# Optimization experiments

Hardware: AMD Instinct MI355X
Metric: run time of the kernel (lower is better)

The kernel has to match this reference:

```python
import jax, jax.numpy as jnp
import numpy as np

ETYPES = [0, 2, 1]          # indexes into doubled RotatE0 r_vec (2*R rows)
OUT_DIM = 64
NUM_HEADS = 8
ALPHA = 0.01                # LeakyReLU slope
R = 2                       # raw relation count (r_vec rows before doubling)
N = 100000                  # num nodes
E = 250000                  # num edges (metapath instances)
L = len(ETYPES) + 1         # metapath length


def setup_inputs() -> dict:
    key = jax.random.key(0)
    k = jax.random.split(key, 6)
    features = jax.random.normal(k[0], (N, OUT_DIM), jnp.float32)
    r_vec = jax.random.normal(k[1], (R, OUT_DIM // 2, 2), jnp.float32)
    attn1_w = jax.random.normal(k[2], (NUM_HEADS, OUT_DIM), jnp.float32) * 0.1
    attn2 = jax.random.normal(k[3], (1, NUM_HEADS, OUT_DIM), jnp.float32) * 0.1
    edge_metapath_indices = jax.random.randint(k[4], (E, L), 0, N)
    edge_dst = jax.random.randint(k[5], (E,), 0, N)
    return {"features": features, "r_vec": r_vec, "attn1_w": attn1_w,
            "attn2": attn2, "edge_metapath_indices": edge_metapath_indices,
            "edge_dst": edge_dst}


def _forward(features, r_vec, attn1_w, attn2, edge_metapath_indices, edge_dst):
    D2 = OUT_DIM // 2
    # --- RotatE0 relation vectors: normalize each complex pair to unit length ---
    rv = r_vec / jnp.linalg.norm(r_vec, axis=2, keepdims=True)      # [R, D2, 2]
    rv_conj = rv * jnp.array([1.0, -1.0], rv.dtype)                 # conjugate
    rv2 = jnp.stack((rv, rv_conj), axis=1).reshape(2 * R, D2, 2)    # [2R, D2, 2]
    # --- cumulative rotation per metapath position (reverse product) ---
    fr = [None] * L
    fr[L - 1] = jnp.stack([jnp.ones(D2, rv.dtype), jnp.zeros(D2, rv.dtype)], -1)
    for i in range(L - 2, -1, -1):
        if ETYPES[i] is not None:
            r = rv2[ETYPES[i]]                                       # [D2, 2]
            re = fr[i + 1][:, 0] * r[:, 0] - fr[i + 1][:, 1] * r[:, 1]
            im = fr[i + 1][:, 0] * r[:, 1] + fr[i + 1][:, 1] * r[:, 0]
            fr[i] = jnp.stack([re, im], axis=-1)
        else:
            fr[i] = fr[i + 1]
    frv = jnp.stack(fr, axis=0)                                      # [L, D2, 2]
    # --- gather node features along each metapath instance ---
    edata = features[edge_metapath_indices]                          # [E, L, D]
    ed = edata.reshape(edata.shape[0], L, D2, 2)
    # position L-1 has identity rotation (1,0), so rotate all positions at once
    re = ed[..., 0] * frv[None, :, :, 0] - ed[..., 1] * frv[None, :, :, 1]
    im = ed[..., 0] * frv[None, :, :, 1] + ed[..., 1] * frv[None, :, :, 0]
    ed = jnp.stack([re, im], axis=-1).reshape(edata.shape[0], L, OUT_DIM)
    hidden = ed.mean(axis=1)                                         # [E, D]
    eft = jnp.tile(hidden, (1, NUM_HEADS)).reshape(-1, NUM_HEADS, OUT_DIM)
    # --- attention scores (attn_switch=True) ---
    center = features[edge_metapath_indices[:, -1]]                  # [E, D]
    a1 = center @ attn1_w.T                                          # [E, H]
    a2 = (eft * attn2).sum(axis=-1)                                  # [E, H]
    a = a1 + a2
    a = jnp.where(a > 0, a, ALPHA * a)[:, :, None]                   # leaky relu, [E,H,1]
    # --- edge softmax over destination-node segments ---
    amax = jax.lax.stop_gradient(jax.ops.segment_max(a, edge_dst, num_segments=N))
    aexp = jnp.exp(a - amax[edge_dst])
    asum = jax.ops.segment_sum(aexp, edge_dst, num_segments=N)
    attn = aexp / asum[edge_dst]                                     # [E, H, 1]
    # --- message passing: weighted scatter-sum to destination nodes ---
    h = jax.ops.segment_sum(eft * attn, edge_dst, num_segments=N)    # [N, H, D]
    return h


def reference(features, r_vec, attn1_w, attn2, edge_metapath_indices, edge_dst):
    return _forward(features, r_vec, attn1_w, attn2, edge_metapath_indices, edge_dst)
```

## Files before the change

kernel.cpp:

```cpp
#include <hip/hip_runtime.h>

#define NUM_HEADS 8

__device__ __forceinline__ float2 cmul(float2 a, float2 b) {
    return make_float2(a.x*b.x - a.y*b.y, a.x*b.y + a.y*b.x);
}

__global__ __launch_bounds__(256) void k_edge(
    const float2* __restrict__ feat,
    const float2* __restrict__ rvec,
    const float2* __restrict__ w1_g,
    const float2* __restrict__ w2_g,
    const int4*   __restrict__ emi,
    const int*    __restrict__ edge_dst,
    float2*       __restrict__ hidden,
    float*        __restrict__ a_buf,
    int*          __restrict__ counts,
    int E)
{
    __shared__ float2 s_frv[96];
    __shared__ float2 s_w1[256];
    __shared__ float2 s_w2[256];
    int tid = threadIdx.x;
    if (tid < 32) {
        float2 a = rvec[tid];
        float2 b = rvec[32 + tid];
        float na = rsqrtf(a.x*a.x + a.y*a.y); a.x *= na; a.y *= na;
        float nb = rsqrtf(b.x*b.x + b.y*b.y); b.x *= nb; b.y *= nb;
        float2 fr2 = make_float2(a.x, -a.y);
        float2 fr1 = cmul(fr2, b);
        float2 fr0 = cmul(fr1, a);
        s_frv[tid] = fr0; s_frv[32+tid] = fr1; s_frv[64+tid] = fr2;
    }
    s_w1[tid] = w1_g[tid];
    s_w2[tid] = w2_g[tid];
    __syncthreads();

    int e = blockIdx.x * 8 + (tid >> 5);
    if (e >= E) return;
    int lane = tid & 31;

    int4 idx = emi[e];
    float2 f0 = feat[(size_t)idx.x * 32 + lane];
    float2 f1 = feat[(size_t)idx.y * 32 + lane];
    float2 f2 = feat[(size_t)idx.z * 32 + lane];
    float2 c3 = feat[(size_t)idx.w * 32 + lane];

    float2 acc = c3;
    float2 q;
    q = s_frv[lane];      acc.x += f0.x*q.x - f0.y*q.y; acc.y += f0.x*q.y + f0.y*q.x;
    q = s_frv[32+lane];   acc.x += f1.x*q.x - f1.y*q.y; acc.y += f1.x*q.y + f1.y*q.x;
    q = s_frv[64+lane];   acc.x += f2.x*q.x - f2.y*q.y; acc.y += f2.x*q.y + f2.y*q.x;
    float2 h = make_float2(acc.x * 0.25f, acc.y * 0.25f);
    hidden[(size_t)e * 32 + lane] = h;

    float p[NUM_HEADS];
    #pragma unroll
    for (int hh = 0; hh < NUM_HEADS; ++hh) {
        float2 w1 = s_w1[hh*32 + lane], w2 = s_w2[hh*32 + lane];
        p[hh] = c3.x*w1.x + c3.y*w1.y + h.x*w2.x + h.y*w2.y;
    }
    float myv = 0.f;
    #pragma unroll
    for (int hh = 0; hh < NUM_HEADS; ++hh) {
        #pragma unroll
        for (int off = 16; off > 0; off >>= 1)
            p[hh] += __shfl_xor(p[hh], off, 32);
        if (lane == hh) myv = p[hh];
    }
    if (lane < NUM_HEADS) {
        float a = myv > 0.f ? myv : 0.01f * myv;
        a_buf[(size_t)e * 8 + lane] = a;
    }
    if (lane == 0) atomicAdd(&counts[edge_dst[e]], 1);
}

__global__ __launch_bounds__(256) void k_scan_a(
    const int* __restrict__ counts, int* __restrict__ offsets,
    int* __restrict__ blocksums, int N)
{
    __shared__ int s[256];
    int t = threadIdx.x;
    int base = blockIdx.x * 1024 + t * 4;
    int v0 = (base     < N) ? counts[base]     : 0;
    int v1 = (base + 1 < N) ? counts[base + 1] : 0;
    int v2 = (base + 2 < N) ? counts[base + 2] : 0;
    int v3 = (base + 3 < N) ? counts[base + 3] : 0;
    s[t] = v0 + v1 + v2 + v3;
    __syncthreads();
    #pragma unroll
    for (int off = 1; off < 256; off <<= 1) {
        int x = (t >= off) ? s[t - off] : 0;
        __syncthreads();
        s[t] += x;
        __syncthreads();
    }
    if (t == 255) blocksums[blockIdx.x] = s[255];
    int run = (t == 0) ? 0 : s[t - 1];
    if (base     < N) offsets[base]     = run; run += v0;
    if (base + 1 < N) offsets[base + 1] = run; run += v1;
    if (base + 2 < N) offsets[base + 2] = run; run += v2;
    if (base + 3 < N) offsets[base + 3] = run;
}

__global__ __launch_bounds__(1024) void k_scan_b(
    int* __restrict__ blocksums, int* __restrict__ total, int B)
{
    __shared__ int s[1024];
    int t = threadIdx.x;
    s[t] = (t < B) ? blocksums[t] : 0;
    __syncthreads();
    #pragma unroll
    for (int off = 1; off < 1024; off <<= 1) {
        int x = (t >= off) ? s[t - off] : 0;
        __syncthreads();
        s[t] += x;
        __syncthreads();
    }
    if (t < B) blocksums[t] = (t == 0) ? 0 : s[t - 1];
    if (t == 1023) *total = s[1023];
}

__global__ __launch_bounds__(256) void k_scan_c(
    int* __restrict__ offsets, int* __restrict__ cursor,
    const int* __restrict__ blocksums, const int* __restrict__ total, int N)
{
    int i = blockIdx.x * 256 + threadIdx.x;
    if (i < N) {
        int v = offsets[i] + blocksums[i >> 10];
        offsets[i] = v;
        cursor[i] = v;
    }
    if (i == 0) offsets[N] = *total;
}

__global__ void k_fill(const int* __restrict__ edge_dst, int* __restrict__ cursor,
                       int* __restrict__ edge_ids, int E) {
    int e = blockIdx.x * 256 + threadIdx.x;
    if (e >= E) return;
    int pos = atomicAdd(&cursor[edge_dst[e]], 1);
    edge_ids[pos] = e;
}

__global__ __launch_bounds__(256) void k_out(
    const float2* __restrict__ hidden,
    const float*  __restrict__ a_buf,
    const int*    __restrict__ offsets,
    const int*    __restrict__ edge_ids,
    float2*       __restrict__ out,
    int N)
{
    int tid = threadIdx.x;
    int n = blockIdx.x * 8 + (tid >> 5);
    if (n >= N) return;
    int lane = tid & 31;
    int beg = offsets[n], end = offsets[n + 1];

    if (beg == end) {
        float2 z = make_float2(0.f, 0.f);
        #pragma unroll
        for (int hh = 0; hh < NUM_HEADS; ++hh)
            out[((size_t)n * 8 + hh) * 32 + lane] = z;
        return;
    }

    const float4* a4 = (const float4*)a_buf;
    float4 m0 = make_float4(-1e30f, -1e30f, -1e30f, -1e30f);
    float4 m1 = m0;
    for (int j = beg; j < end; ++j) {
        int e = edge_ids[j];
        float4 x0 = a4[(size_t)e * 2], x1 = a4[(size_t)e * 2 + 1];
        m0.x = fmaxf(m0.x, x0.x); m0.y = fmaxf(m0.y, x0.y);
        m0.z = fmaxf(m0.z, x0.z); m0.w = fmaxf(m0.w, x0.w);
        m1.x = fmaxf(m1.x, x1.x); m1.y = fmaxf(m1.y, x1.y);
        m1.z = fmaxf(m1.z, x1.z); m1.w = fmaxf(m1.w, x1.w);
    }
    float4 d0 = make_float4(0.f, 0.f, 0.f, 0.f), d1 = d0;
    float2 acc[NUM_HEADS];
    #pragma unroll
    for (int hh = 0; hh < NUM_HEADS; ++hh) acc[hh] = make_float2(0.f, 0.f);
    for (int j = beg; j < end; ++j) {
        int e = edge_ids[j];
        float4 x0 = a4[(size_t)e * 2], x1 = a4[(size_t)e * 2 + 1];
        float w0x = __expf(x0.x - m0.x), w0y = __expf(x0.y - m0.y);
        float w0z = __expf(x0.z - m0.z), w0w = __expf(x0.w - m0.w);
        float w1x = __expf(x1.x - m1.x), w1y = __expf(x1.y - m1.y);
        float w1z = __expf(x1.z - m1.z), w1w = __expf(x1.w - m1.w);
        d0.x += w0x; d0.y += w0y; d0.z += w0z; d0.w += w0w;
        d1.x += w1x; d1.y += w1y; d1.z += w1z; d1.w += w1w;
        float2 hv = hidden[(size_t)e * 32 + lane];
        acc[0].x += hv.x * w0x; acc[0].y += hv.y * w0x;
        acc[1].x += hv.x * w0y; acc[1].y += hv.y * w0y;
        acc[2].x += hv.x * w0z; acc[2].y += hv.y * w0z;
        acc[3].x += hv.x * w0w; acc[3].y += hv.y * w0w;
        acc[4].x += hv.x * w1x; acc[4].y += hv.y * w1x;
        acc[5].x += hv.x * w1y; acc[5].y += hv.y * w1y;
        acc[6].x += hv.x * w1z; acc[6].y += hv.y * w1z;
        acc[7].x += hv.x * w1w; acc[7].y += hv.y * w1w;
    }
    float r[NUM_HEADS] = {1.f/d0.x, 1.f/d0.y, 1.f/d0.z, 1.f/d0.w,
                          1.f/d1.x, 1.f/d1.y, 1.f/d1.z, 1.f/d1.w};
    #pragma unroll
    for (int hh = 0; hh < NUM_HEADS; ++hh) {
        float2 v = make_float2(acc[hh].x * r[hh], acc[hh].y * r[hh]);
        out[((size_t)n * 8 + hh) * 32 + lane] = v;
    }
}

extern "C" void kernel_launch(void* const* d_in, const int* in_sizes, int n_in,
                              void* d_out, int out_size, void* d_ws, size_t ws_size,
                              hipStream_t stream) {
    const float2* feat = (const float2*)d_in[0];
    const float2* rvec = (const float2*)d_in[1];
    const float2* w1   = (const float2*)d_in[2];
    const float2* w2   = (const float2*)d_in[3];
    const int4*   emi  = (const int4*)d_in[4];
    const int* edge_dst = (const int*)d_in[5];

    int N = in_sizes[0] / 64;
    int E = in_sizes[4] / 4;
    int nTiles = (N + 1023) / 1024;

    char* w = (char*)d_ws;
    float*    hidden   = (float*)w;
    float*    a_buf    = hidden + (size_t)E * 64;
    int*      counts   = (int*)(a_buf + (size_t)E * 8);
    int*      offsets  = counts + N;
    int*      cursor   = offsets + N + 1;
    int*      edge_ids = cursor + N;
    int*      blocksums= edge_ids + E;
    int*      total    = blocksums + 1024;

    hipMemsetAsync(counts, 0, (size_t)N * 4, stream);

    k_edge<<<(E + 7) / 8, 256, 0, stream>>>(feat, rvec, w1, w2, emi, edge_dst,
                                            (float2*)hidden, a_buf, counts, E);
    k_scan_a<<<nTiles, 256, 0, stream>>>(counts, offsets, blocksums, N);
    k_scan_b<<<1, 1024, 0, stream>>>(blocksums, total, nTiles);
    k_scan_c<<<(N + 255) / 256, 256, 0, stream>>>(offsets, cursor, blocksums, total, N);
    k_fill<<<(E + 255) / 256, 256, 0, stream>>>(edge_dst, cursor, edge_ids, E);
    k_out<<<(N + 7) / 8, 256, 0, stream>>>((const float2*)hidden, a_buf,
                                           offsets, edge_ids, (float2*)d_out, N);
}
```

Measured before the change: 376.4 us.

## Precompute per-node attention projections and fuse edge computation into the CSR gather kernel

```diff
diff --git a/kernel.cpp b/kernel.cpp
--- a/kernel.cpp
+++ b/kernel.cpp
@@ -6,73 +6,51 @@
     return make_float2(a.x*b.x - a.y*b.y, a.x*b.y + a.y*b.x);
 }
 
-__global__ __launch_bounds__(256) void k_edge(
+__global__ __launch_bounds__(256) void k_pre(
     const float2* __restrict__ feat,
     const float2* __restrict__ rvec,
     const float2* __restrict__ w1_g,
     const float2* __restrict__ w2_g,
-    const int4*   __restrict__ emi,
-    const int*    __restrict__ edge_dst,
-    float2*       __restrict__ hidden,
-    float*        __restrict__ a_buf,
-    int*          __restrict__ counts,
-    int E)
-{
-    __shared__ float2 s_frv[96];
-    __shared__ float2 s_w1[256];
-    __shared__ float2 s_w2[256];
+    float*        __restrict__ P, int N)
+{
     int tid = threadIdx.x;
-    if (tid < 32) {
-        float2 a = rvec[tid];
-        float2 b = rvec[32 + tid];
+    int lane = tid & 31;
+    int l = lane >> 3, h = lane & 7;
+
+    float2 Wr[32];
+    for (int d = 0; d < 32; ++d) {
+        float2 a = rvec[d], b = rvec[32 + d];
         float na = rsqrtf(a.x*a.x + a.y*a.y); a.x *= na; a.y *= na;
         float nb = rsqrtf(b.x*b.x + b.y*b.y); b.x *= nb; b.y *= nb;
         float2 fr2 = make_float2(a.x, -a.y);
         float2 fr1 = cmul(fr2, b);
         float2 fr0 = cmul(fr1, a);
-        s_frv[tid] = fr0; s_frv[32+tid] = fr1; s_frv[64+tid] = fr2;
-    }
-    s_w1[tid] = w1_g[tid];
-    s_w2[tid] = w2_g[tid];
-    __syncthreads();
-
-    int e = blockIdx.x * 8 + (tid >> 5);
-    if (e >= E) return;
-    int lane = tid & 31;
-
-    int4 idx = emi[e];
-    float2 f0 = feat[(size_t)idx.x * 32 + lane];
-    float2 f1 = feat[(size_t)idx.y * 32 + lane];
-    float2 f2 = feat[(size_t)idx.z * 32 + lane];
-    float2 c3 = feat[(size_t)idx.w * 32 + lane];
-
-    float2 acc = c3;
-    float2 q;
-    q = s_frv[lane];      acc.x += f0.x*q.x - f0.y*q.y; acc.y += f0.x*q.y + f0.y*q.x;
-    q = s_frv[32+lane];   acc.x += f1.x*q.x - f1.y*q.y; acc.y += f1.x*q.y + f1.y*q.x;
-    q = s_frv[64+lane];   acc.x += f2.x*q.x - f2.y*q.y; acc.y += f2.x*q.y + f2.y*q.x;
-    float2 h = make_float2(acc.x * 0.25f, acc.y * 0.25f);
-    hidden[(size_t)e * 32 + lane] = h;
-
-    float p[NUM_HEADS];
-    #pragma unroll
-    for (int hh = 0; hh < NUM_HEADS; ++hh) {
-        float2 w1 = s_w1[hh*32 + lane], w2 = s_w2[hh*32 + lane];
-        p[hh] = c3.x*w1.x + c3.y*w1.y + h.x*w2.x + h.y*w2.y;
-    }
-    float myv = 0.f;
-    #pragma unroll
-    for (int hh = 0; hh < NUM_HEADS; ++hh) {
+        float2 fr = (l == 0) ? fr0 : (l == 1) ? fr1 : (l == 2) ? fr2 : make_float2(1.f, 0.f);
+        float2 frc = make_float2(fr.x, -fr.y);
+        float2 w2 = w2_g[h*32 + d];
+        float2 wl = cmul(w2, frc);
+        wl.x *= 0.25f; wl.y *= 0.25f;
+        if (l == 3) { float2 w1 = w1_g[h*32 + d]; wl.x += w1.x; wl.y += w1.y; }
+        Wr[d] = wl;
+    }
+
+    int g = tid >> 5;
+    for (int n = blockIdx.x * 8 + g; n < N; n += gridDim.x * 8) {
+        const float4* f4 = (const float4*)(feat + (size_t)n * 32);
+        float acc = 0.f;
         #pragma unroll
-        for (int off = 16; off > 0; off >>= 1)
-            p[hh] += __shfl_xor(p[hh], off, 32);
-        if (lane == hh) myv = p[hh];
-    }
-    if (lane < NUM_HEADS) {
-        float a = myv > 0.f ? myv : 0.01f * myv;
-        a_buf[(size_t)e * 8 + lane] = a;
-    }
-    if (lane == 0) atomicAdd(&counts[edge_dst[e]], 1);
+        for (int q = 0; q < 16; ++q) {
+            float4 v = f4[q];
+            acc += v.x * Wr[2*q].x + v.y * Wr[2*q].y
+                 + v.z * Wr[2*q+1].x + v.w * Wr[2*q+1].y;
+        }
+        P[(size_t)n * 32 + lane] = acc;
+    }
+}
+
+__global__ void k_count(const int* __restrict__ edge_dst, int* __restrict__ counts, int E) {
+    int e = blockIdx.x * 256 + threadIdx.x;
+    if (e < E) atomicAdd(&counts[edge_dst[e]], 1);
 }
 
 __global__ __launch_bounds__(256) void k_scan_a(
@@ -135,22 +113,35 @@
 }
 
 __global__ void k_fill(const int* __restrict__ edge_dst, int* __restrict__ cursor,
-                       int* __restrict__ edge_ids, int E) {
+                       const int4* __restrict__ emi, int4* __restrict__ emi_perm, int E) {
     int e = blockIdx.x * 256 + threadIdx.x;
     if (e >= E) return;
     int pos = atomicAdd(&cursor[edge_dst[e]], 1);
-    edge_ids[pos] = e;
+    emi_perm[pos] = emi[e];
 }
 
 __global__ __launch_bounds__(256) void k_out(
-    const float2* __restrict__ hidden,
-    const float*  __restrict__ a_buf,
+    const float2* __restrict__ feat,
+    const float2* __restrict__ rvec,
+    const float*  __restrict__ P,
     const int*    __restrict__ offsets,
-    const int*    __restrict__ edge_ids,
+    const int4*   __restrict__ emi_perm,
     float2*       __restrict__ out,
     int N)
 {
+    __shared__ float2 s_frv[96];
     int tid = threadIdx.x;
+    if (tid < 32) {
+        float2 a = rvec[tid], b = rvec[32 + tid];
+        float na = rsqrtf(a.x*a.x + a.y*a.y); a.x *= na; a.y *= na;
+        float nb = rsqrtf(b.x*b.x + b.y*b.y); b.x *= nb; b.y *= nb;
+        float2 fr2 = make_float2(a.x, -a.y);
+        float2 fr1 = cmul(fr2, b);
+        float2 fr0 = cmul(fr1, a);
+        s_frv[tid] = fr0; s_frv[32 + tid] = fr1; s_frv[64 + tid] = fr2;
+    }
+    __syncthreads();
+
     int n = blockIdx.x * 8 + (tid >> 5);
     if (n >= N) return;
     int lane = tid & 31;
@@ -164,46 +155,62 @@
         return;
     }
 
-    const float4* a4 = (const float4*)a_buf;
-    float4 m0 = make_float4(-1e30f, -1e30f, -1e30f, -1e30f);
-    float4 m1 = m0;
+    float2 fr0 = s_frv[lane], fr1 = s_frv[32 + lane], fr2 = s_frv[64 + lane];
+
+    float dsum[NUM_HEADS];
+    float2 acc[NUM_HEADS];
+    #pragma unroll
+    for (int hh = 0; hh < NUM_HEADS; ++hh) { dsum[hh] = 0.f; acc[hh] = make_float2(0.f, 0.f); }
+
     for (int j = beg; j < end; ++j) {
-        int e = edge_ids[j];
-        float4 x0 = a4[(size_t)e * 2], x1 = a4[(size_t)e * 2 + 1];
-        m0.x = fmaxf(m0.x, x0.x); m0.y = fmaxf(m0.y, x0.y);
-        m0.z = fmaxf(m0.z, x0.z); m0.w = fmaxf(m0.w, x0.w);
-        m1.x = fmaxf(m1.x, x1.x); m1.y = fmaxf(m1.y, x1.y);
-        m1.z = fmaxf(m1.z, x1.z); m1.w = fmaxf(m1.w, x1.w);
-    }
-    float4 d0 = make_float4(0.f, 0.f, 0.f, 0.f), d1 = d0;
-    float2 acc[NUM_HEADS];
-    #pragma unroll
-    for (int hh = 0; hh < NUM_HEADS; ++hh) acc[hh] = make_float2(0.f, 0.f);
-    for (int j = beg; j < end; ++j) {
-        int e = edge_ids[j];
-        float4 x0 = a4[(size_t)e * 2], x1 = a4[(size_t)e * 2 + 1];
-        float w0x = __expf(x0.x - m0.x), w0y = __expf(x0.y - m0.y);
-        float w0z = __expf(x0.z - m0.z), w0w = __expf(x0.w - m0.w);
-        float w1x = __expf(x1.x - m1.x), w1y = __expf(x1.y - m1.y);
-        float w1z = __expf(x1.z - m1.z), w1w = __expf(x1.w - m1.w);
-        d0.x += w0x; d0.y += w0y; d0.z += w0z; d0.w += w0w;
-        d1.x += w1x; d1.y += w1y; d1.z += w1z; d1.w += w1w;
-        float2 hv = hidden[(size_t)e * 32 + lane];
-        acc[0].x += hv.x * w0x; acc[0].y += hv.y * w0x;
-        acc[1].x += hv.x * w0y; acc[1].y += hv.y * w0y;
-        acc[2].x += hv.x * w0z; acc[2].y += hv.y * w0z;
-        acc[3].x += hv.x * w0w; acc[3].y += hv.y * w0w;
-        acc[4].x += hv.x * w1x; acc[4].y += hv.y * w1x;
-        acc[5].x += hv.x * w1y; acc[5].y += hv.y * w1y;
-        acc[6].x += hv.x * w1z; acc[6].y += hv.y * w1z;
-        acc[7].x += hv.x * w1w; acc[7].y += hv.y * w1w;
-    }
-    float r[NUM_HEADS] = {1.f/d0.x, 1.f/d0.y, 1.f/d0.z, 1.f/d0.w,
-                          1.f/d1.x, 1.f/d1.y, 1.f/d1.z, 1.f/d1.w};
+        int4 idx = emi_perm[j];
+
+        const float4* q0 = (const float4*)(P + (size_t)idx.x * 32);
+        const float4* q1 = (const float4*)(P + (size_t)idx.y * 32 + 8);
+        const float4* q2 = (const float4*)(P + (size_t)idx.z * 32 + 16);
+        const float4* q3 = (const float4*)(P + (size_t)idx.w * 32 + 24);
+        float4 u0 = q0[0], v0 = q0[1];
+        float4 u1 = q1[0], v1 = q1[1];
+        float4 u2 = q2[0], v2 = q2[1];
+        float4 u3 = q3[0], v3 = q3[1];
+        float aw[NUM_HEADS];
+        aw[0] = u0.x + u1.x + u2.x + u3.x;
+        aw[1] = u0.y + u1.y + u2.y + u3.y;
+        aw[2] = u0.z + u1.z + u2.z + u3.z;
+        aw[3] = u0.w + u1.w + u2.w + u3.w;
+        aw[4] = v0.x + v1.x + v2.x + v3.x;
+        aw[5] = v0.y + v1.y + v2.y + v3.y;
+        aw[6] = v0.z + v1.z + v2.z + v3.z;
+        aw[7] = v0.w + v1.w + v2.w + v3.w;
+
+        float2 f0 = feat[(size_t)idx.x * 32 + lane];
+        float2 f1 = feat[(size_t)idx.y * 32 + lane];
+        float2 f2 = feat[(size_t)idx.z * 32 + lane];
+        float2 c3 = feat[(size_t)idx.w * 32 + lane];
+        float2 hv;
+        hv.x = c3.x + f0.x*fr0.x - f0.y*fr0.y
+                    + f1.x*fr1.x - f1.y*fr1.y
+                    + f2.x*fr2.x - f2.y*fr2.y;
+        hv.y = c3.y + f0.x*fr0.y + f0.y*fr0.x
+                    + f1.x*fr1.y + f1.y*fr1.x
+                    + f2.x*fr2.y + f2.y*fr2.x;
+        hv.x *= 0.25f; hv.y *= 0.25f;
+
+        #pragma unroll
+        for (int hh = 0; hh < NUM_HEADS; ++hh) {
+            float av = aw[hh];
+            av = av > 0.f ? av : 0.01f * av;
+            float wgt = __expf(av);
+            dsum[hh] += wgt;
+            acc[hh].x += wgt * hv.x;
+            acc[hh].y += wgt * hv.y;
+        }
+    }
+
     #pragma unroll
     for (int hh = 0; hh < NUM_HEADS; ++hh) {
-        float2 v = make_float2(acc[hh].x * r[hh], acc[hh].y * r[hh]);
-        out[((size_t)n * 8 + hh) * 32 + lane] = v;
+        float r = 1.f / dsum[hh];
+        out[((size_t)n * 8 + hh) * 32 + lane] = make_float2(acc[hh].x * r, acc[hh].y * r);
     }
 }
 
@@ -222,23 +229,22 @@
     int nTiles = (N + 1023) / 1024;
 
     char* w = (char*)d_ws;
-    float*    hidden   = (float*)w;
-    float*    a_buf    = hidden + (size_t)E * 64;
-    int*      counts   = (int*)(a_buf + (size_t)E * 8);
-    int*      offsets  = counts + N;
-    int*      cursor   = offsets + N + 1;
-    int*      edge_ids = cursor + N;
-    int*      blocksums= edge_ids + E;
-    int*      total    = blocksums + 1024;
+    float* P        = (float*)w;
+    int4*  emi_perm = (int4*)(P + (size_t)N * 32);
+    int*   counts   = (int*)(emi_perm + E);
+    int*   offsets  = counts + N;
+    int*   cursor   = offsets + N + 1;
+    int*   blocksums= cursor + N;
+    int*   total    = blocksums + 1024;
 
     hipMemsetAsync(counts, 0, (size_t)N * 4, stream);
 
-    k_edge<<<(E + 7) / 8, 256, 0, stream>>>(feat, rvec, w1, w2, emi, edge_dst,
-                                            (float2*)hidden, a_buf, counts, E);
+    k_count<<<(E + 255) / 256, 256, 0, stream>>>(edge_dst, counts, E);
+    k_pre<<<(N + 63) / 64, 256, 0, stream>>>(feat, rvec, w1, w2, P, N);
     k_scan_a<<<nTiles, 256, 0, stream>>>(counts, offsets, blocksums, N);
     k_scan_b<<<1, 1024, 0, stream>>>(blocksums, total, nTiles);
     k_scan_c<<<(N + 255) / 256, 256, 0, stream>>>(offsets, cursor, blocksums, total, N);
-    k_fill<<<(E + 255) / 256, 256, 0, stream>>>(edge_dst, cursor, edge_ids, E);
-    k_out<<<(N + 7) / 8, 256, 0, stream>>>((const float2*)hidden, a_buf,
-                                           offsets, edge_ids, (float2*)d_out, N);
-}
+    k_fill<<<(E + 255) / 256, 256, 0, stream>>>(edge_dst, cursor, emi, emi_perm, E);
+    k_out<<<(N + 7) / 8, 256, 0, stream>>>(feat, rvec, P, offsets, emi_perm,
+                                           (float2*)d_out, N);
+}
```

New measurement: 394.0 us. +4.7%, slower.
